# Optimization experiments

Hardware: AMD Instinct MI355X
Metric: run time of the kernel (lower is better)

The kernel has to match this reference:

```python
import jax, jax.numpy as jnp
import numpy as np

NUM_ANCHORS = 5
NUM_CLASSES = 20


def setup_inputs() -> dict:
    key = jax.random.key(0)
    k1, k2, k3, k4 = jax.random.split(key, 4)
    N, H, W, M = 64, 52, 52, 32
    img = 1664
    x = jax.random.normal(k1, (N, NUM_ANCHORS * (5 + NUM_CLASSES), H, W), jnp.float32)
    anchors = jnp.array([[1.08, 1.19], [3.42, 4.41], [6.63, 11.38],
                         [9.42, 5.11], [16.62, 10.52]], jnp.float32)
    # valid gt boxes in xyxy pixel coords
    xy = jax.random.uniform(k2, (N, M, 2), jnp.float32) * (img * 0.8)
    wh = jax.random.uniform(k3, (N, M, 2), jnp.float32) * (img * 0.2) + 1.0
    gt_boxes = jnp.concatenate([xy, xy + wh], axis=-1)
    gt_labels = jax.random.randint(k4, (N, M), 0, NUM_CLASSES)
    return dict(x=x, anchors=anchors, gt_boxes=gt_boxes, gt_labels=gt_labels,
                img_h=img, img_w=img)


def _format_outputs(x, anchors, img_h, img_w):
    # x: [N, A*(5+C), H, W] -> (coords [N,HW,A,4] (x,y,w,h), obj [N,HW,A], scores [N,HW,A,C])
    N, _, H, W = x.shape
    A = anchors.shape[0]
    t = x.reshape(N, A, 5 + NUM_CLASSES, H, W).transpose(0, 3, 4, 1, 2)  # [N,H,W,A,5+C]
    c_x = jnp.arange(W, dtype=x.dtype) * (img_w / W)
    c_y = jnp.arange(H, dtype=x.dtype) * (img_h / H)
    b_x = jax.nn.sigmoid(t[..., 0]) + c_x[None, None, :, None]   # [N,H,W,A]
    b_y = jax.nn.sigmoid(t[..., 1]) + c_y[None, :, None, None]
    b_w = (img_w / W) * anchors[:, 0] * jnp.exp(t[..., 2])
    b_h = (img_h / H) * anchors[:, 1] * jnp.exp(t[..., 3])
    coords = jnp.stack([b_x, b_y, b_w, b_h], axis=-1).reshape(N, H * W, A, 4)
    b_o = jax.nn.sigmoid(t[..., 4]).reshape(N, H * W, A)
    scores = t[..., 5:].reshape(N, H * W, A, NUM_CLASSES)
    return coords, b_o, scores


def reference(x, anchors, gt_boxes, gt_labels, img_h, img_w):
    coords, b_o, scores = _format_outputs(x, anchors, img_h, img_w)
    # pred_boxes[..., 2:] += pred_boxes[..., :2]  (xywh -> xyxy)
    boxes = jnp.concatenate([coords[..., :2], coords[..., :2] + coords[..., 2:]], axis=-1)  # [N,HW,A,4]
    # box_iou: pred [N,HW,A,1,4] vs gt [N,1,1,M,4] -> [N,HW,A,M]
    p = boxes[..., None, :]
    g = gt_boxes[:, None, None, :, :]
    lt = jnp.maximum(p[..., :2], g[..., :2])
    rb = jnp.minimum(p[..., 2:], g[..., 2:])
    whi = jnp.clip(rb - lt, 0.0)
    inter = whi[..., 0] * whi[..., 1]
    area_p = (boxes[..., 2] - boxes[..., 0]) * (boxes[..., 3] - boxes[..., 1])
    area_g = (gt_boxes[..., 2] - gt_boxes[..., 0]) * (gt_boxes[..., 3] - gt_boxes[..., 1])
    iou = inter / (area_p[..., None] + area_g[:, None, None, :] - inter)   # [N,HW,A,M]

    cell_sel = iou.max(axis=(2, 3)) > 0.0                 # [N,HW]
    best_a = jnp.argmax(iou.max(axis=3), axis=2)          # [N,HW] best anchor per cell
    iou_best = jnp.take_along_axis(iou, best_a[..., None, None], axis=2)[:, :, 0, :]  # [N,HW,M]
    max_iou = iou_best.max(axis=-1)                       # [N,HW]
    gt_idx = jnp.argmax(iou_best, axis=-1)                # [N,HW]

    sel_box = jnp.take_along_axis(boxes, best_a[..., None, None], axis=2)[:, :, 0, :]   # [N,HW,4]
    sel_o = jnp.take_along_axis(b_o, best_a[..., None], axis=2)[:, :, 0]                # [N,HW]
    sel_sc = jnp.take_along_axis(scores, best_a[..., None, None], axis=2)[:, :, 0, :]   # [N,HW,C]
    g_box = jnp.take_along_axis(gt_boxes, gt_idx[..., None], axis=1)                    # [N,HW,4]
    g_lab = jnp.take_along_axis(gt_labels, gt_idx, axis=1)                              # [N,HW]

    m = cell_sel.astype(x.dtype)
    objectness_loss = (jnp.sum(m * (sel_o - max_iou) ** 2)
                       + 0.5 * jnp.sum((1.0 - m) * b_o.max(axis=2) ** 2))
    bbox_loss = (jnp.sum(m * jnp.sum((sel_box[..., :2] - g_box[..., :2]) ** 2, axis=-1))
                 + jnp.sum(m * jnp.sum((jnp.sqrt(sel_box[..., 2:]) - jnp.sqrt(g_box[..., 2:])) ** 2, axis=-1)))
    logp = jax.nn.log_softmax(sel_sc, axis=-1)
    ce = -jnp.take_along_axis(logp, g_lab[..., None], axis=-1)[..., 0]
    clf_loss = jnp.sum(m * ce)
    return jnp.stack([objectness_loss, bbox_loss, clf_loss])
```

## Files before the change

kernel.cpp:

```cpp
#include <hip/hip_runtime.h>
#include <math.h>

#define A_ 5
#define C_ 20
#define N_ 64
#define H_ 52
#define W_ 52
#define HW_ (H_ * W_)
#define M_ 32
#define CH_ (A_ * (5 + C_))
#define CPB 64
#define NBLK_X ((HW_ + CPB - 1) / CPB)
#define NBLK (NBLK_X * N_)

__global__ __launch_bounds__(320) void yolo_main(
    const float* __restrict__ x,
    const float* __restrict__ anchors,
    const float* __restrict__ gt,
    const int* __restrict__ glab,
    const void* img_h_p, const void* img_w_p,
    float* __restrict__ ws)
{
    __shared__ float s_c[5][A_][CPB];

    const int tid  = threadIdx.x;
    const int a    = tid >> 6;
    const int lane = tid & 63;
    const int n    = blockIdx.y;
    const int cell = blockIdx.x * CPB + lane;
    const bool valid = cell < HW_;

    int ibw = *(const int*)img_w_p;
    float img_w = (ibw > 0 && ibw < 1000000) ? (float)ibw : *(const float*)img_w_p;
    int ibh = *(const int*)img_h_p;
    float img_h = (ibh > 0 && ibh < 1000000) ? (float)ibh : *(const float*)img_h_p;
    const float sx = img_w / (float)W_;
    const float sy = img_h / (float)H_;

    const float ax = anchors[2 * a];
    const float ay = anchors[2 * a + 1];

    float bi = 0.f, bu = 1.f;
    int   bm = 0;
    float ov = 0.f, ce = 0.f, bb = 0.f;

    if (valid) {
        const int wi = cell % W_;
        const int hi = cell / W_;
        const size_t base = (size_t)n * CH_ * HW_ + (size_t)a * 25 * HW_ + cell;
        float t0 = x[base];
        float t1 = x[base + (size_t)HW_];
        float t2 = x[base + 2 * (size_t)HW_];
        float t3 = x[base + 3 * (size_t)HW_];
        float t4 = x[base + 4 * (size_t)HW_];
        float sc[C_];
        #pragma unroll
        for (int j = 0; j < C_; ++j)
            sc[j] = x[base + (size_t)(5 + j) * HW_];

        float bx = 1.f / (1.f + __expf(-t0)) + (float)wi * sx;
        float by = 1.f / (1.f + __expf(-t1)) + (float)hi * sy;
        float bw = sx * ax * __expf(t2);
        float bh = sy * ay * __expf(t3);
        float x1 = bx, y1 = by, x2 = bx + bw, y2 = by + bh;
        ov = 1.f / (1.f + __expf(-t4));
        float ap = (x2 - x1) * (y2 - y1);

        const float4* gtv = (const float4*)(gt + (size_t)n * M_ * 4);
        #pragma unroll 8
        for (int m = 0; m < M_; ++m) {
            float4 g = gtv[m];
            float area = (g.z - g.x) * (g.w - g.y);
            float wxi = fminf(x2, g.z) - fmaxf(x1, g.x);
            float hyi = fminf(y2, g.w) - fmaxf(y1, g.y);
            wxi = fmaxf(wxi, 0.f);
            hyi = fmaxf(hyi, 0.f);
            float inter = wxi * hyi;
            float uni = ap + area - inter;
            if (inter * bu > bi * uni) { bi = inter; bu = uni; bm = m; }
        }

        float4 g = ((const float4*)gt)[n * M_ + bm];
        int lab = glab[n * M_ + bm];
        float d0 = x1 - g.x;
        float d1 = y1 - g.y;
        float d2 = sqrtf(x2) - sqrtf(g.z);
        float d3 = sqrtf(y2) - sqrtf(g.w);
        bb = d0 * d0 + d1 * d1 + d2 * d2 + d3 * d3;

        float mx = sc[0];
        #pragma unroll
        for (int j = 1; j < C_; ++j) mx = fmaxf(mx, sc[j]);
        float se = 0.f, scl = sc[0];
        #pragma unroll
        for (int j = 0; j < C_; ++j) {
            se += __expf(sc[j] - mx);
            scl = (j == lab) ? sc[j] : scl;
        }
        ce = mx + __logf(se) - scl;
    }

    s_c[0][a][lane] = bi;
    s_c[1][a][lane] = bu;
    s_c[2][a][lane] = ov;
    s_c[3][a][lane] = ce;
    s_c[4][a][lane] = bb;
    __syncthreads();

    if (tid < 64) {
        float Bi = 0.f, Bu = 1.f, O = 0.f, CE = 0.f, BB = 0.f;
        float bomax = -1e30f;
        #pragma unroll
        for (int aa = 0; aa < A_; ++aa) {
            float ci = s_c[0][aa][lane];
            float cu = s_c[1][aa][lane];
            float co = s_c[2][aa][lane];
            bomax = fmaxf(bomax, co);
            bool upd = (aa == 0) || (ci * Bu > Bi * cu);
            if (upd) {
                Bi = ci; Bu = cu; O = co;
                CE = s_c[3][aa][lane];
                BB = s_c[4][aa][lane];
            }
        }

        float obj = 0.f, bbx = 0.f, clf = 0.f;
        if (valid) {
            if (Bi > 0.f) {
                float d = O - Bi / Bu;
                obj = d * d;
                bbx = BB;
                clf = CE;
            } else {
                obj = 0.5f * bomax * bomax;
            }
        }

        #pragma unroll
        for (int off = 32; off > 0; off >>= 1) {
            obj += __shfl_down(obj, off, 64);
            bbx += __shfl_down(bbx, off, 64);
            clf += __shfl_down(clf, off, 64);
        }
        if (tid == 0) {
            const int bid = blockIdx.y * gridDim.x + blockIdx.x;
            ws[0 * NBLK + bid] = obj;
            ws[1 * NBLK + bid] = bbx;
            ws[2 * NBLK + bid] = clf;
        }
    }
}

__global__ __launch_bounds__(1024) void yolo_reduce(
    const float* __restrict__ ws, float* __restrict__ out)
{
    __shared__ float s_red[16][3];
    const int tid = threadIdx.x;
    float o = 0.f, b = 0.f, c = 0.f;
    for (int e = tid; e < NBLK; e += 1024) {
        o += ws[0 * NBLK + e];
        b += ws[1 * NBLK + e];
        c += ws[2 * NBLK + e];
    }
    #pragma unroll
    for (int off = 32; off > 0; off >>= 1) {
        o += __shfl_down(o, off, 64);
        b += __shfl_down(b, off, 64);
        c += __shfl_down(c, off, 64);
    }
    const int wid = tid >> 6;
    if ((tid & 63) == 0) {
        s_red[wid][0] = o; s_red[wid][1] = b; s_red[wid][2] = c;
    }
    __syncthreads();
    if (tid == 0) {
        float oo = 0.f, bb = 0.f, cc = 0.f;
        #pragma unroll
        for (int w = 0; w < 16; ++w) {
            oo += s_red[w][0]; bb += s_red[w][1]; cc += s_red[w][2];
        }
        out[0] = oo; out[1] = bb; out[2] = cc;
    }
}

extern "C" void kernel_launch(void* const* d_in, const int* in_sizes, int n_in,
                              void* d_out, int out_size, void* d_ws, size_t ws_size,
                              hipStream_t stream) {
    (void)in_sizes; (void)n_in; (void)out_size; (void)ws_size;
    const float* x    = (const float*)d_in[0];
    const float* anch = (const float*)d_in[1];
    const float* gt   = (const float*)d_in[2];
    const int*   gl   = (const int*)d_in[3];
    const void*  ih   = d_in[4];
    const void*  iw   = d_in[5];
    float* out = (float*)d_out;
    float* ws  = (float*)d_ws;

    dim3 grid(NBLK_X, N_);
    yolo_main<<<grid, dim3(320), 0, stream>>>(x, anch, gt, gl, ih, iw, ws);
    yolo_reduce<<<1, 1024, 0, stream>>>(ws, out);
}
```

Before: 143.3 us.

## Process four cells per thread with float4 loads and 256-cell blocks

Each thread now handles four consecutive cells, loading all 25 anchor channels as float4 vectors, and each block covers 256 cells instead of 64. One GT box read now serves four IoU updates. The target-class logit is re-read from global memory instead of selected from registers, and the final reduce uses all five waves. The aim is fewer, wider memory transactions and less per-cell overhead, at the cost of higher register pressure (float4 S[20]) and fewer blocks in the grid. HW=2704 is divisible by 4, so the vector loads stay aligned.

```diff
diff --git a/kernel.cpp b/kernel.cpp
--- a/kernel.cpp
+++ b/kernel.cpp
@@ -9,11 +9,11 @@
 #define HW_ (H_ * W_)
 #define M_ 32
 #define CH_ (A_ * (5 + C_))
-#define CPB 64
+#define CPB 256
 #define NBLK_X ((HW_ + CPB - 1) / CPB)
 #define NBLK (NBLK_X * N_)
 
-__global__ __launch_bounds__(320) void yolo_main(
+__global__ __launch_bounds__(320, 3) void yolo_main(
     const float* __restrict__ x,
     const float* __restrict__ anchors,
     const float* __restrict__ gt,
@@ -27,8 +27,8 @@
     const int a    = tid >> 6;
     const int lane = tid & 63;
     const int n    = blockIdx.y;
-    const int cell = blockIdx.x * CPB + lane;
-    const bool valid = cell < HW_;
+    const int cb   = blockIdx.x * CPB + lane * 4;
+    const bool valid = cb < HW_;
 
     int ibw = *(const int*)img_w_p;
     float img_w = (ibw > 0 && ibw < 1000000) ? (float)ibw : *(const float*)img_w_p;
@@ -40,114 +40,157 @@
     const float ax = anchors[2 * a];
     const float ay = anchors[2 * a + 1];
 
-    float bi = 0.f, bu = 1.f;
-    int   bm = 0;
-    float ov = 0.f, ce = 0.f, bb = 0.f;
+    float bi[4] = {0.f, 0.f, 0.f, 0.f};
+    float bu[4] = {1.f, 1.f, 1.f, 1.f};
+    int   bm[4] = {0, 0, 0, 0};
+    float ov[4] = {0.f, 0.f, 0.f, 0.f};
+    float ce[4] = {0.f, 0.f, 0.f, 0.f};
+    float bb[4] = {0.f, 0.f, 0.f, 0.f};
 
     if (valid) {
-        const int wi = cell % W_;
-        const int hi = cell / W_;
-        const size_t base = (size_t)n * CH_ * HW_ + (size_t)a * 25 * HW_ + cell;
-        float t0 = x[base];
-        float t1 = x[base + (size_t)HW_];
-        float t2 = x[base + 2 * (size_t)HW_];
-        float t3 = x[base + 3 * (size_t)HW_];
-        float t4 = x[base + 4 * (size_t)HW_];
-        float sc[C_];
+        const size_t base = (size_t)n * CH_ * HW_ + (size_t)a * 25 * HW_ + cb;
+
+        float4 S[C_];
         #pragma unroll
         for (int j = 0; j < C_; ++j)
-            sc[j] = x[base + (size_t)(5 + j) * HW_];
-
-        float bx = 1.f / (1.f + __expf(-t0)) + (float)wi * sx;
-        float by = 1.f / (1.f + __expf(-t1)) + (float)hi * sy;
-        float bw = sx * ax * __expf(t2);
-        float bh = sy * ay * __expf(t3);
-        float x1 = bx, y1 = by, x2 = bx + bw, y2 = by + bh;
-        ov = 1.f / (1.f + __expf(-t4));
-        float ap = (x2 - x1) * (y2 - y1);
+            S[j] = *(const float4*)(x + base + (size_t)(5 + j) * HW_);
+        float4 T0 = *(const float4*)(x + base);
+        float4 T1 = *(const float4*)(x + base + (size_t)HW_);
+        float4 T2 = *(const float4*)(x + base + 2 * (size_t)HW_);
+        float4 T3 = *(const float4*)(x + base + 3 * (size_t)HW_);
+        float4 T4 = *(const float4*)(x + base + 4 * (size_t)HW_);
+
+        float lse[4];
+        {
+            const float* Sf = (const float*)S;
+            #pragma unroll
+            for (int k = 0; k < 4; ++k) {
+                float mx = Sf[k];
+                #pragma unroll
+                for (int j = 1; j < C_; ++j) mx = fmaxf(mx, Sf[j * 4 + k]);
+                float se = 0.f;
+                #pragma unroll
+                for (int j = 0; j < C_; ++j) se += __expf(Sf[j * 4 + k] - mx);
+                lse[k] = mx + __logf(se);
+            }
+        }
+
+        float x1[4], y1[4], x2[4], y2[4], ap[4];
+        {
+            const float* t0 = (const float*)&T0;
+            const float* t1 = (const float*)&T1;
+            const float* t2 = (const float*)&T2;
+            const float* t3 = (const float*)&T3;
+            const float* t4 = (const float*)&T4;
+            #pragma unroll
+            for (int k = 0; k < 4; ++k) {
+                const int c  = cb + k;
+                const int wi = c % W_;
+                const int hi = c / W_;
+                float bx = 1.f / (1.f + __expf(-t0[k])) + (float)wi * sx;
+                float by = 1.f / (1.f + __expf(-t1[k])) + (float)hi * sy;
+                float bw = sx * ax * __expf(t2[k]);
+                float bh = sy * ay * __expf(t3[k]);
+                x1[k] = bx; y1[k] = by; x2[k] = bx + bw; y2[k] = by + bh;
+                ov[k] = 1.f / (1.f + __expf(-t4[k]));
+                ap[k] = (x2[k] - x1[k]) * (y2[k] - y1[k]);
+            }
+        }
 
         const float4* gtv = (const float4*)(gt + (size_t)n * M_ * 4);
-        #pragma unroll 8
+        #pragma unroll 4
         for (int m = 0; m < M_; ++m) {
             float4 g = gtv[m];
             float area = (g.z - g.x) * (g.w - g.y);
-            float wxi = fminf(x2, g.z) - fmaxf(x1, g.x);
-            float hyi = fminf(y2, g.w) - fmaxf(y1, g.y);
-            wxi = fmaxf(wxi, 0.f);
-            hyi = fmaxf(hyi, 0.f);
-            float inter = wxi * hyi;
-            float uni = ap + area - inter;
-            if (inter * bu > bi * uni) { bi = inter; bu = uni; bm = m; }
-        }
-
-        float4 g = ((const float4*)gt)[n * M_ + bm];
-        int lab = glab[n * M_ + bm];
-        float d0 = x1 - g.x;
-        float d1 = y1 - g.y;
-        float d2 = sqrtf(x2) - sqrtf(g.z);
-        float d3 = sqrtf(y2) - sqrtf(g.w);
-        bb = d0 * d0 + d1 * d1 + d2 * d2 + d3 * d3;
-
-        float mx = sc[0];
-        #pragma unroll
-        for (int j = 1; j < C_; ++j) mx = fmaxf(mx, sc[j]);
-        float se = 0.f, scl = sc[0];
-        #pragma unroll
-        for (int j = 0; j < C_; ++j) {
-            se += __expf(sc[j] - mx);
-            scl = (j == lab) ? sc[j] : scl;
-        }
-        ce = mx + __logf(se) - scl;
-    }
-
-    s_c[0][a][lane] = bi;
-    s_c[1][a][lane] = bu;
-    s_c[2][a][lane] = ov;
-    s_c[3][a][lane] = ce;
-    s_c[4][a][lane] = bb;
+            #pragma unroll
+            for (int k = 0; k < 4; ++k) {
+                float wxi = fminf(x2[k], g.z) - fmaxf(x1[k], g.x);
+                float hyi = fminf(y2[k], g.w) - fmaxf(y1[k], g.y);
+                wxi = fmaxf(wxi, 0.f);
+                hyi = fmaxf(hyi, 0.f);
+                float inter = wxi * hyi;
+                float uni = ap[k] + area - inter;
+                if (inter * bu[k] > bi[k] * uni) { bi[k] = inter; bu[k] = uni; bm[k] = m; }
+            }
+        }
+
+        #pragma unroll
+        for (int k = 0; k < 4; ++k) {
+            float4 g = ((const float4*)gt)[n * M_ + bm[k]];
+            int lab = glab[n * M_ + bm[k]];
+            float d0 = x1[k] - g.x;
+            float d1 = y1[k] - g.y;
+            float d2 = sqrtf(x2[k]) - sqrtf(g.z);
+            float d3 = sqrtf(y2[k]) - sqrtf(g.w);
+            bb[k] = d0 * d0 + d1 * d1 + d2 * d2 + d3 * d3;
+            float sval = x[base + (size_t)(5 + lab) * HW_ + k];
+            ce[k] = lse[k] - sval;
+        }
+    }
+
+    if (valid) {
+        const int cl = lane * 4;
+        #pragma unroll
+        for (int k = 0; k < 4; ++k) {
+            s_c[0][a][cl + k] = bi[k];
+            s_c[1][a][cl + k] = bu[k];
+            s_c[2][a][cl + k] = ov[k];
+            s_c[3][a][cl + k] = ce[k];
+            s_c[4][a][cl + k] = bb[k];
+        }
+    }
     __syncthreads();
 
-    if (tid < 64) {
+    float obj = 0.f, bbx = 0.f, clf = 0.f;
+    if (tid < 256 && (blockIdx.x * CPB + tid) < HW_) {
+        const int t = tid;
         float Bi = 0.f, Bu = 1.f, O = 0.f, CE = 0.f, BB = 0.f;
         float bomax = -1e30f;
         #pragma unroll
         for (int aa = 0; aa < A_; ++aa) {
-            float ci = s_c[0][aa][lane];
-            float cu = s_c[1][aa][lane];
-            float co = s_c[2][aa][lane];
+            float ci = s_c[0][aa][t];
+            float cu = s_c[1][aa][t];
+            float co = s_c[2][aa][t];
             bomax = fmaxf(bomax, co);
             bool upd = (aa == 0) || (ci * Bu > Bi * cu);
             if (upd) {
                 Bi = ci; Bu = cu; O = co;
-                CE = s_c[3][aa][lane];
-                BB = s_c[4][aa][lane];
-            }
-        }
-
-        float obj = 0.f, bbx = 0.f, clf = 0.f;
-        if (valid) {
-            if (Bi > 0.f) {
-                float d = O - Bi / Bu;
-                obj = d * d;
-                bbx = BB;
-                clf = CE;
-            } else {
-                obj = 0.5f * bomax * bomax;
-            }
-        }
-
-        #pragma unroll
-        for (int off = 32; off > 0; off >>= 1) {
-            obj += __shfl_down(obj, off, 64);
-            bbx += __shfl_down(bbx, off, 64);
-            clf += __shfl_down(clf, off, 64);
-        }
-        if (tid == 0) {
-            const int bid = blockIdx.y * gridDim.x + blockIdx.x;
-            ws[0 * NBLK + bid] = obj;
-            ws[1 * NBLK + bid] = bbx;
-            ws[2 * NBLK + bid] = clf;
-        }
+                CE = s_c[3][aa][t];
+                BB = s_c[4][aa][t];
+            }
+        }
+        if (Bi > 0.f) {
+            float d = O - Bi / Bu;
+            obj = d * d;
+            bbx = BB;
+            clf = CE;
+        } else {
+            obj = 0.5f * bomax * bomax;
+        }
+    }
+
+    #pragma unroll
+    for (int off = 32; off > 0; off >>= 1) {
+        obj += __shfl_down(obj, off, 64);
+        bbx += __shfl_down(bbx, off, 64);
+        clf += __shfl_down(clf, off, 64);
+    }
+    __shared__ float s_red[5][3];
+    if ((tid & 63) == 0) {
+        const int wid = tid >> 6;
+        s_red[wid][0] = obj; s_red[wid][1] = bbx; s_red[wid][2] = clf;
+    }
+    __syncthreads();
+    if (tid == 0) {
+        float oo = 0.f, bs = 0.f, cc = 0.f;
+        #pragma unroll
+        for (int w = 0; w < 5; ++w) {
+            oo += s_red[w][0]; bs += s_red[w][1]; cc += s_red[w][2];
+        }
+        const int bid = blockIdx.y * gridDim.x + blockIdx.x;
+        ws[0 * NBLK + bid] = oo;
+        ws[1 * NBLK + bid] = bs;
+        ws[2 * NBLK + bid] = cc;
     }
 }
 
```

After: 159.0 us. 1.11x slower.

## Split into pair IoU kernel and per-cell loss kernel, loading class scores only for best anchor

Applied to the files above, without the earlier changes.

The fused kernel is split in two. The first kernel computes, for each cell and anchor, the decoded box and the best ground-truth IoU from only the five box and objectness channels, and writes intersection, union, objectness and match index to the workspace. The second kernel runs one thread per cell: it picks the best anchor, then reloads the box channels and 20 class scores only for that anchor and only when a match exists. This avoids reading every anchor's class scores and drops the shared-memory anchor reduction, at the cost of about 14 MB of workspace written and read back, an extra launch, and recomputing the winning anchor's box decode.

```diff
diff --git a/kernel.cpp b/kernel.cpp
--- a/kernel.cpp
+++ b/kernel.cpp
@@ -9,11 +9,79 @@
 #define HW_ (H_ * W_)
 #define M_ 32
 #define CH_ (A_ * (5 + C_))
-#define CPB 64
-#define NBLK_X ((HW_ + CPB - 1) / CPB)
-#define NBLK (NBLK_X * N_)
-
-__global__ __launch_bounds__(320) void yolo_main(
+#define PAIRS (N_ * A_ * HW_)
+#define CPB_A 64
+#define NBX_A ((HW_ + CPB_A - 1) / CPB_A)
+#define CPB_B 256
+#define NBX_B ((HW_ + CPB_B - 1) / CPB_B)
+#define NBLK_B (NBX_B * N_)
+#define WS_PART (4 * (size_t)PAIRS)
+
+__global__ __launch_bounds__(320) void yolo_pair(
+    const float* __restrict__ x,
+    const float* __restrict__ anchors,
+    const float* __restrict__ gt,
+    const void* img_h_p, const void* img_w_p,
+    float* __restrict__ ws)
+{
+    const int tid  = threadIdx.x;
+    const int a    = tid >> 6;
+    const int lane = tid & 63;
+    const int n    = blockIdx.y;
+    const int cell = blockIdx.x * CPB_A + lane;
+    if (cell >= HW_) return;
+
+    int ibw = *(const int*)img_w_p;
+    float img_w = (ibw > 0 && ibw < 1000000) ? (float)ibw : *(const float*)img_w_p;
+    int ibh = *(const int*)img_h_p;
+    float img_h = (ibh > 0 && ibh < 1000000) ? (float)ibh : *(const float*)img_h_p;
+    const float sx = img_w / (float)W_;
+    const float sy = img_h / (float)H_;
+
+    const float ax = anchors[2 * a];
+    const float ay = anchors[2 * a + 1];
+
+    const int wi = cell % W_;
+    const int hi = cell / W_;
+    const size_t base = (size_t)n * CH_ * HW_ + (size_t)a * 25 * HW_ + cell;
+    float t0 = x[base];
+    float t1 = x[base + (size_t)HW_];
+    float t2 = x[base + 2 * (size_t)HW_];
+    float t3 = x[base + 3 * (size_t)HW_];
+    float t4 = x[base + 4 * (size_t)HW_];
+
+    float bx = 1.f / (1.f + __expf(-t0)) + (float)wi * sx;
+    float by = 1.f / (1.f + __expf(-t1)) + (float)hi * sy;
+    float bw = sx * ax * __expf(t2);
+    float bh = sy * ay * __expf(t3);
+    float x1 = bx, y1 = by, x2 = bx + bw, y2 = by + bh;
+    float ov = 1.f / (1.f + __expf(-t4));
+    float ap = (x2 - x1) * (y2 - y1);
+
+    float bi = 0.f, bu = 1.f;
+    int   bm = 0;
+    const float4* gtv = (const float4*)(gt + (size_t)n * M_ * 4);
+    #pragma unroll 8
+    for (int m = 0; m < M_; ++m) {
+        float4 g = gtv[m];
+        float area = (g.z - g.x) * (g.w - g.y);
+        float wxi = fminf(x2, g.z) - fmaxf(x1, g.x);
+        float hyi = fminf(y2, g.w) - fmaxf(y1, g.y);
+        wxi = fmaxf(wxi, 0.f);
+        hyi = fmaxf(hyi, 0.f);
+        float inter = wxi * hyi;
+        float uni = ap + area - inter;
+        if (inter * bu > bi * uni) { bi = inter; bu = uni; bm = m; }
+    }
+
+    const size_t o = ((size_t)(n * A_ + a)) * HW_ + cell;
+    ws[0 * (size_t)PAIRS + o] = bi;
+    ws[1 * (size_t)PAIRS + o] = bu;
+    ws[2 * (size_t)PAIRS + o] = ov;
+    ws[3 * (size_t)PAIRS + o] = __int_as_float(bm);
+}
+
+__global__ __launch_bounds__(256) void yolo_cell(
     const float* __restrict__ x,
     const float* __restrict__ anchors,
     const float* __restrict__ gt,
@@ -21,133 +89,106 @@
     const void* img_h_p, const void* img_w_p,
     float* __restrict__ ws)
 {
-    __shared__ float s_c[5][A_][CPB];
-
     const int tid  = threadIdx.x;
-    const int a    = tid >> 6;
-    const int lane = tid & 63;
     const int n    = blockIdx.y;
-    const int cell = blockIdx.x * CPB + lane;
+    const int cell = blockIdx.x * CPB_B + tid;
     const bool valid = cell < HW_;
 
-    int ibw = *(const int*)img_w_p;
-    float img_w = (ibw > 0 && ibw < 1000000) ? (float)ibw : *(const float*)img_w_p;
-    int ibh = *(const int*)img_h_p;
-    float img_h = (ibh > 0 && ibh < 1000000) ? (float)ibh : *(const float*)img_h_p;
-    const float sx = img_w / (float)W_;
-    const float sy = img_h / (float)H_;
-
-    const float ax = anchors[2 * a];
-    const float ay = anchors[2 * a + 1];
-
-    float bi = 0.f, bu = 1.f;
-    int   bm = 0;
-    float ov = 0.f, ce = 0.f, bb = 0.f;
+    float obj = 0.f, bbx = 0.f, clf = 0.f;
 
     if (valid) {
-        const int wi = cell % W_;
-        const int hi = cell / W_;
-        const size_t base = (size_t)n * CH_ * HW_ + (size_t)a * 25 * HW_ + cell;
-        float t0 = x[base];
-        float t1 = x[base + (size_t)HW_];
-        float t2 = x[base + 2 * (size_t)HW_];
-        float t3 = x[base + 3 * (size_t)HW_];
-        float t4 = x[base + 4 * (size_t)HW_];
-        float sc[C_];
-        #pragma unroll
-        for (int j = 0; j < C_; ++j)
-            sc[j] = x[base + (size_t)(5 + j) * HW_];
-
-        float bx = 1.f / (1.f + __expf(-t0)) + (float)wi * sx;
-        float by = 1.f / (1.f + __expf(-t1)) + (float)hi * sy;
-        float bw = sx * ax * __expf(t2);
-        float bh = sy * ay * __expf(t3);
-        float x1 = bx, y1 = by, x2 = bx + bw, y2 = by + bh;
-        ov = 1.f / (1.f + __expf(-t4));
-        float ap = (x2 - x1) * (y2 - y1);
-
-        const float4* gtv = (const float4*)(gt + (size_t)n * M_ * 4);
-        #pragma unroll 8
-        for (int m = 0; m < M_; ++m) {
-            float4 g = gtv[m];
-            float area = (g.z - g.x) * (g.w - g.y);
-            float wxi = fminf(x2, g.z) - fmaxf(x1, g.x);
-            float hyi = fminf(y2, g.w) - fmaxf(y1, g.y);
-            wxi = fmaxf(wxi, 0.f);
-            hyi = fmaxf(hyi, 0.f);
-            float inter = wxi * hyi;
-            float uni = ap + area - inter;
-            if (inter * bu > bi * uni) { bi = inter; bu = uni; bm = m; }
-        }
-
-        float4 g = ((const float4*)gt)[n * M_ + bm];
-        int lab = glab[n * M_ + bm];
-        float d0 = x1 - g.x;
-        float d1 = y1 - g.y;
-        float d2 = sqrtf(x2) - sqrtf(g.z);
-        float d3 = sqrtf(y2) - sqrtf(g.w);
-        bb = d0 * d0 + d1 * d1 + d2 * d2 + d3 * d3;
-
-        float mx = sc[0];
-        #pragma unroll
-        for (int j = 1; j < C_; ++j) mx = fmaxf(mx, sc[j]);
-        float se = 0.f, scl = sc[0];
-        #pragma unroll
-        for (int j = 0; j < C_; ++j) {
-            se += __expf(sc[j] - mx);
-            scl = (j == lab) ? sc[j] : scl;
-        }
-        ce = mx + __logf(se) - scl;
-    }
-
-    s_c[0][a][lane] = bi;
-    s_c[1][a][lane] = bu;
-    s_c[2][a][lane] = ov;
-    s_c[3][a][lane] = ce;
-    s_c[4][a][lane] = bb;
-    __syncthreads();
-
-    if (tid < 64) {
-        float Bi = 0.f, Bu = 1.f, O = 0.f, CE = 0.f, BB = 0.f;
+        int ibw = *(const int*)img_w_p;
+        float img_w = (ibw > 0 && ibw < 1000000) ? (float)ibw : *(const float*)img_w_p;
+        int ibh = *(const int*)img_h_p;
+        float img_h = (ibh > 0 && ibh < 1000000) ? (float)ibh : *(const float*)img_h_p;
+        const float sx = img_w / (float)W_;
+        const float sy = img_h / (float)H_;
+
+        const size_t bp = ((size_t)(n * A_)) * HW_ + cell;
+        float Bi = 0.f, Bu = 1.f, O = 0.f;
+        int Ba = 0, Bm = 0;
         float bomax = -1e30f;
         #pragma unroll
-        for (int aa = 0; aa < A_; ++aa) {
-            float ci = s_c[0][aa][lane];
-            float cu = s_c[1][aa][lane];
-            float co = s_c[2][aa][lane];
+        for (int a = 0; a < A_; ++a) {
+            float ci = ws[0 * (size_t)PAIRS + bp + (size_t)a * HW_];
+            float cu = ws[1 * (size_t)PAIRS + bp + (size_t)a * HW_];
+            float co = ws[2 * (size_t)PAIRS + bp + (size_t)a * HW_];
             bomax = fmaxf(bomax, co);
-            bool upd = (aa == 0) || (ci * Bu > Bi * cu);
+            bool upd = (a == 0) || (ci * Bu > Bi * cu);
             if (upd) {
-                Bi = ci; Bu = cu; O = co;
-                CE = s_c[3][aa][lane];
-                BB = s_c[4][aa][lane];
+                Bi = ci; Bu = cu; O = co; Ba = a;
+                Bm = __float_as_int(ws[3 * (size_t)PAIRS + bp + (size_t)a * HW_]);
             }
         }
 
-        float obj = 0.f, bbx = 0.f, clf = 0.f;
-        if (valid) {
-            if (Bi > 0.f) {
-                float d = O - Bi / Bu;
-                obj = d * d;
-                bbx = BB;
-                clf = CE;
-            } else {
-                obj = 0.5f * bomax * bomax;
+        if (Bi > 0.f) {
+            float d = O - Bi / Bu;
+            obj = d * d;
+
+            const size_t xb = (size_t)n * CH_ * HW_ + (size_t)(Ba * 25) * HW_ + cell;
+            float t0 = x[xb];
+            float t1 = x[xb + (size_t)HW_];
+            float t2 = x[xb + 2 * (size_t)HW_];
+            float t3 = x[xb + 3 * (size_t)HW_];
+            const int wi = cell % W_;
+            const int hi = cell / W_;
+            float ax = anchors[2 * Ba];
+            float ay = anchors[2 * Ba + 1];
+            float bx = 1.f / (1.f + __expf(-t0)) + (float)wi * sx;
+            float by = 1.f / (1.f + __expf(-t1)) + (float)hi * sy;
+            float bw = sx * ax * __expf(t2);
+            float bh = sy * ay * __expf(t3);
+            float x1 = bx, y1 = by, x2 = bx + bw, y2 = by + bh;
+
+            float4 g = ((const float4*)gt)[n * M_ + Bm];
+            int lab = glab[n * M_ + Bm];
+            float d0 = x1 - g.x;
+            float d1 = y1 - g.y;
+            float d2 = sqrtf(x2) - sqrtf(g.z);
+            float d3 = sqrtf(y2) - sqrtf(g.w);
+            bbx = d0 * d0 + d1 * d1 + d2 * d2 + d3 * d3;
+
+            float sc[C_];
+            #pragma unroll
+            for (int j = 0; j < C_; ++j)
+                sc[j] = x[xb + (size_t)(5 + j) * HW_];
+            float mx = sc[0];
+            #pragma unroll
+            for (int j = 1; j < C_; ++j) mx = fmaxf(mx, sc[j]);
+            float se = 0.f, scl = sc[0];
+            #pragma unroll
+            for (int j = 0; j < C_; ++j) {
+                se += __expf(sc[j] - mx);
+                scl = (j == lab) ? sc[j] : scl;
             }
-        }
-
+            clf = mx + __logf(se) - scl;
+        } else {
+            obj = 0.5f * bomax * bomax;
+        }
+    }
+
+    #pragma unroll
+    for (int off = 32; off > 0; off >>= 1) {
+        obj += __shfl_down(obj, off, 64);
+        bbx += __shfl_down(bbx, off, 64);
+        clf += __shfl_down(clf, off, 64);
+    }
+    __shared__ float s_red[4][3];
+    if ((tid & 63) == 0) {
+        const int wid = tid >> 6;
+        s_red[wid][0] = obj; s_red[wid][1] = bbx; s_red[wid][2] = clf;
+    }
+    __syncthreads();
+    if (tid == 0) {
+        float oo = 0.f, bs = 0.f, cc = 0.f;
         #pragma unroll
-        for (int off = 32; off > 0; off >>= 1) {
-            obj += __shfl_down(obj, off, 64);
-            bbx += __shfl_down(bbx, off, 64);
-            clf += __shfl_down(clf, off, 64);
-        }
-        if (tid == 0) {
-            const int bid = blockIdx.y * gridDim.x + blockIdx.x;
-            ws[0 * NBLK + bid] = obj;
-            ws[1 * NBLK + bid] = bbx;
-            ws[2 * NBLK + bid] = clf;
-        }
+        for (int w = 0; w < 4; ++w) {
+            oo += s_red[w][0]; bs += s_red[w][1]; cc += s_red[w][2];
+        }
+        const int bid = blockIdx.y * gridDim.x + blockIdx.x;
+        ws[WS_PART + 0 * NBLK_B + bid] = oo;
+        ws[WS_PART + 1 * NBLK_B + bid] = bs;
+        ws[WS_PART + 2 * NBLK_B + bid] = cc;
     }
 }
 
@@ -157,10 +198,10 @@
     __shared__ float s_red[16][3];
     const int tid = threadIdx.x;
     float o = 0.f, b = 0.f, c = 0.f;
-    for (int e = tid; e < NBLK; e += 1024) {
-        o += ws[0 * NBLK + e];
-        b += ws[1 * NBLK + e];
-        c += ws[2 * NBLK + e];
+    if (tid < NBLK_B) {
+        o = ws[WS_PART + 0 * NBLK_B + tid];
+        b = ws[WS_PART + 1 * NBLK_B + tid];
+        c = ws[WS_PART + 2 * NBLK_B + tid];
     }
     #pragma unroll
     for (int off = 32; off > 0; off >>= 1) {
@@ -196,7 +237,9 @@
     float* out = (float*)d_out;
     float* ws  = (float*)d_ws;
 
-    dim3 grid(NBLK_X, N_);
-    yolo_main<<<grid, dim3(320), 0, stream>>>(x, anch, gt, gl, ih, iw, ws);
+    dim3 gridA(NBX_A, N_);
+    yolo_pair<<<gridA, dim3(320), 0, stream>>>(x, anch, gt, ih, iw, ws);
+    dim3 gridB(NBX_B, N_);
+    yolo_cell<<<gridB, dim3(CPB_B), 0, stream>>>(x, anch, gt, gl, ih, iw, ws);
     yolo_reduce<<<1, 1024, 0, stream>>>(ws, out);
 }
```

New measurement: 162.2 us. 13.2% more time.

## Process all anchors per thread and load class scores only for selected anchor

Applied to the files above, without the earlier changes.

Restructures the main kernel so each thread evaluates all five anchors for its cell instead of one wavefront per anchor. The best anchor is now chosen in registers rather than through shared memory. Class logits are loaded and softmaxed only for the winning anchor of positive cells, which cuts global memory reads substantially. The costs are more registers per thread and smaller 64-thread blocks, which may reduce latency hiding.

```diff
diff --git a/kernel.cpp b/kernel.cpp
--- a/kernel.cpp
+++ b/kernel.cpp
@@ -10,10 +10,10 @@
 #define M_ 32
 #define CH_ (A_ * (5 + C_))
 #define CPB 64
-#define NBLK_X ((HW_ + CPB - 1) / CPB)
-#define NBLK (NBLK_X * N_)
+#define NBX ((HW_ + CPB - 1) / CPB)
+#define NBLK (NBX * N_)
 
-__global__ __launch_bounds__(320) void yolo_main(
+__global__ __launch_bounds__(64) void yolo_main(
     const float* __restrict__ x,
     const float* __restrict__ anchors,
     const float* __restrict__ gt,
@@ -21,11 +21,7 @@
     const void* img_h_p, const void* img_w_p,
     float* __restrict__ ws)
 {
-    __shared__ float s_c[5][A_][CPB];
-
-    const int tid  = threadIdx.x;
-    const int a    = tid >> 6;
-    const int lane = tid & 63;
+    const int lane = threadIdx.x;
     const int n    = blockIdx.y;
     const int cell = blockIdx.x * CPB + lane;
     const bool valid = cell < HW_;
@@ -37,117 +33,114 @@
     const float sx = img_w / (float)W_;
     const float sy = img_h / (float)H_;
 
-    const float ax = anchors[2 * a];
-    const float ay = anchors[2 * a + 1];
-
-    float bi = 0.f, bu = 1.f;
-    int   bm = 0;
-    float ov = 0.f, ce = 0.f, bb = 0.f;
+    float obj = 0.f, bbx = 0.f, clf = 0.f;
 
     if (valid) {
+        const size_t base = (size_t)n * CH_ * HW_ + cell;
+
+        float t[A_][5];
+        #pragma unroll
+        for (int a = 0; a < A_; ++a)
+            #pragma unroll
+            for (int v = 0; v < 5; ++v)
+                t[a][v] = x[base + (size_t)(a * 25 + v) * HW_];
+
         const int wi = cell % W_;
         const int hi = cell / W_;
-        const size_t base = (size_t)n * CH_ * HW_ + (size_t)a * 25 * HW_ + cell;
-        float t0 = x[base];
-        float t1 = x[base + (size_t)HW_];
-        float t2 = x[base + 2 * (size_t)HW_];
-        float t3 = x[base + 3 * (size_t)HW_];
-        float t4 = x[base + 4 * (size_t)HW_];
-        float sc[C_];
+
+        float X1[A_], Y1[A_], X2[A_], Y2[A_], AP[A_], OVv[A_];
         #pragma unroll
-        for (int j = 0; j < C_; ++j)
-            sc[j] = x[base + (size_t)(5 + j) * HW_];
+        for (int a = 0; a < A_; ++a) {
+            float ax = anchors[2 * a];
+            float ay = anchors[2 * a + 1];
+            float bx = 1.f / (1.f + __expf(-t[a][0])) + (float)wi * sx;
+            float by = 1.f / (1.f + __expf(-t[a][1])) + (float)hi * sy;
+            float bw = sx * ax * __expf(t[a][2]);
+            float bh = sy * ay * __expf(t[a][3]);
+            X1[a] = bx; Y1[a] = by; X2[a] = bx + bw; Y2[a] = by + bh;
+            AP[a] = (X2[a] - X1[a]) * (Y2[a] - Y1[a]);
+            OVv[a] = 1.f / (1.f + __expf(-t[a][4]));
+        }
 
-        float bx = 1.f / (1.f + __expf(-t0)) + (float)wi * sx;
-        float by = 1.f / (1.f + __expf(-t1)) + (float)hi * sy;
-        float bw = sx * ax * __expf(t2);
-        float bh = sy * ay * __expf(t3);
-        float x1 = bx, y1 = by, x2 = bx + bw, y2 = by + bh;
-        ov = 1.f / (1.f + __expf(-t4));
-        float ap = (x2 - x1) * (y2 - y1);
-
+        float BIv[A_] = {0.f, 0.f, 0.f, 0.f, 0.f};
+        float BUv[A_] = {1.f, 1.f, 1.f, 1.f, 1.f};
+        int   BMv[A_] = {0, 0, 0, 0, 0};
         const float4* gtv = (const float4*)(gt + (size_t)n * M_ * 4);
         #pragma unroll 8
         for (int m = 0; m < M_; ++m) {
             float4 g = gtv[m];
             float area = (g.z - g.x) * (g.w - g.y);
-            float wxi = fminf(x2, g.z) - fmaxf(x1, g.x);
-            float hyi = fminf(y2, g.w) - fmaxf(y1, g.y);
-            wxi = fmaxf(wxi, 0.f);
-            hyi = fmaxf(hyi, 0.f);
-            float inter = wxi * hyi;
-            float uni = ap + area - inter;
-            if (inter * bu > bi * uni) { bi = inter; bu = uni; bm = m; }
-        }
-
-        float4 g = ((const float4*)gt)[n * M_ + bm];
-        int lab = glab[n * M_ + bm];
-        float d0 = x1 - g.x;
-        float d1 = y1 - g.y;
-        float d2 = sqrtf(x2) - sqrtf(g.z);
-        float d3 = sqrtf(y2) - sqrtf(g.w);
-        bb = d0 * d0 + d1 * d1 + d2 * d2 + d3 * d3;
-
-        float mx = sc[0];
-        #pragma unroll
-        for (int j = 1; j < C_; ++j) mx = fmaxf(mx, sc[j]);
-        float se = 0.f, scl = sc[0];
-        #pragma unroll
-        for (int j = 0; j < C_; ++j) {
-            se += __expf(sc[j] - mx);
-            scl = (j == lab) ? sc[j] : scl;
-        }
-        ce = mx + __logf(se) - scl;
-    }
-
-    s_c[0][a][lane] = bi;
-    s_c[1][a][lane] = bu;
-    s_c[2][a][lane] = ov;
-    s_c[3][a][lane] = ce;
-    s_c[4][a][lane] = bb;
-    __syncthreads();
-
-    if (tid < 64) {
-        float Bi = 0.f, Bu = 1.f, O = 0.f, CE = 0.f, BB = 0.f;
-        float bomax = -1e30f;
-        #pragma unroll
-        for (int aa = 0; aa < A_; ++aa) {
-            float ci = s_c[0][aa][lane];
-            float cu = s_c[1][aa][lane];
-            float co = s_c[2][aa][lane];
-            bomax = fmaxf(bomax, co);
-            bool upd = (aa == 0) || (ci * Bu > Bi * cu);
-            if (upd) {
-                Bi = ci; Bu = cu; O = co;
-                CE = s_c[3][aa][lane];
-                BB = s_c[4][aa][lane];
+            #pragma unroll
+            for (int a = 0; a < A_; ++a) {
+                float wq = fminf(X2[a], g.z) - fmaxf(X1[a], g.x);
+                float hq = fminf(Y2[a], g.w) - fmaxf(Y1[a], g.y);
+                wq = fmaxf(wq, 0.f);
+                hq = fmaxf(hq, 0.f);
+                float inter = wq * hq;
+                float uni = AP[a] + area - inter;
+                if (inter * BUv[a] > BIv[a] * uni) {
+                    BIv[a] = inter; BUv[a] = uni; BMv[a] = m;
+                }
             }
         }
 
-        float obj = 0.f, bbx = 0.f, clf = 0.f;
-        if (valid) {
-            if (Bi > 0.f) {
-                float d = O - Bi / Bu;
-                obj = d * d;
-                bbx = BB;
-                clf = CE;
-            } else {
-                obj = 0.5f * bomax * bomax;
+        float Bi = BIv[0], Bu = BUv[0], O = OVv[0];
+        float wx1 = X1[0], wy1 = Y1[0], wx2 = X2[0], wy2 = Y2[0];
+        int Ba = 0, Bm = BMv[0];
+        float bomax = OVv[0];
+        #pragma unroll
+        for (int a = 1; a < A_; ++a) {
+            bomax = fmaxf(bomax, OVv[a]);
+            if (BIv[a] * Bu > Bi * BUv[a]) {
+                Bi = BIv[a]; Bu = BUv[a]; O = OVv[a];
+                wx1 = X1[a]; wy1 = Y1[a]; wx2 = X2[a]; wy2 = Y2[a];
+                Ba = a; Bm = BMv[a];
             }
         }
 
-        #pragma unroll
-        for (int off = 32; off > 0; off >>= 1) {
-            obj += __shfl_down(obj, off, 64);
-            bbx += __shfl_down(bbx, off, 64);
-            clf += __shfl_down(clf, off, 64);
+        if (Bi > 0.f) {
+            float d = O - Bi / Bu;
+            obj = d * d;
+
+            float4 g = ((const float4*)gt)[n * M_ + Bm];
+            int lab = glab[n * M_ + Bm];
+            float d0 = wx1 - g.x;
+            float d1 = wy1 - g.y;
+            float d2 = sqrtf(wx2) - sqrtf(g.z);
+            float d3 = sqrtf(wy2) - sqrtf(g.w);
+            bbx = d0 * d0 + d1 * d1 + d2 * d2 + d3 * d3;
+
+            const size_t sb = base + (size_t)(Ba * 25 + 5) * HW_;
+            float sc[C_];
+            #pragma unroll
+            for (int j = 0; j < C_; ++j)
+                sc[j] = x[sb + (size_t)j * HW_];
+            float mx = sc[0];
+            #pragma unroll
+            for (int j = 1; j < C_; ++j) mx = fmaxf(mx, sc[j]);
+            float se = 0.f, scl = sc[0];
+            #pragma unroll
+            for (int j = 0; j < C_; ++j) {
+                se += __expf(sc[j] - mx);
+                scl = (j == lab) ? sc[j] : scl;
+            }
+            clf = mx + __logf(se) - scl;
+        } else {
+            obj = 0.5f * bomax * bomax;
         }
-        if (tid == 0) {
-            const int bid = blockIdx.y * gridDim.x + blockIdx.x;
-            ws[0 * NBLK + bid] = obj;
-            ws[1 * NBLK + bid] = bbx;
-            ws[2 * NBLK + bid] = clf;
-        }
+    }
+
+    #pragma unroll
+    for (int off = 32; off > 0; off >>= 1) {
+        obj += __shfl_down(obj, off, 64);
+        bbx += __shfl_down(bbx, off, 64);
+        clf += __shfl_down(clf, off, 64);
+    }
+    if (lane == 0) {
+        const int bid = blockIdx.y * gridDim.x + blockIdx.x;
+        ws[0 * NBLK + bid] = obj;
+        ws[1 * NBLK + bid] = bbx;
+        ws[2 * NBLK + bid] = clf;
     }
 }
 
@@ -196,7 +189,7 @@
     float* out = (float*)d_out;
     float* ws  = (float*)d_ws;
 
-    dim3 grid(NBLK_X, N_);
-    yolo_main<<<grid, dim3(320), 0, stream>>>(x, anch, gt, gl, ih, iw, ws);
+    dim3 grid(NBX, N_);
+    yolo_main<<<grid, dim3(64), 0, stream>>>(x, anch, gt, gl, ih, iw, ws);
     yolo_reduce<<<1, 1024, 0, stream>>>(ws, out);
 }
```

Result: no change. 141.1 us (median of 2 runs) (-1.6%).
